# Optimization experiments

Measured on AMD Instinct MI355X. Metric: run time of the kernel, lower is better.

The kernel has to match this reference:

```python
import jax, jax.numpy as jnp
import numpy as np

NUM_LAYERS = 5
EMB = 300
N_GRAPHS = 4096
BN_EPS = 1e-5
TEMP = 0.04


def _gnn_encode(x, edge_index, edge_attr, atom_emb1, atom_emb2,
                edge_emb1, edge_emb2, mlp_w1, mlp_b1, mlp_w2, mlp_b2,
                bn_gamma, bn_beta):
    n = x.shape[0]
    h = atom_emb1[x[:, 0]] + atom_emb2[x[:, 1]]  # [N, EMB]
    src, dst = edge_index[0], edge_index[1]
    for l in range(NUM_LAYERS):
        eemb = edge_emb1[l][edge_attr[:, 0]] + edge_emb2[l][edge_attr[:, 1]]  # [E, EMB]
        self_emb = edge_emb1[l][4] + edge_emb2[l][0]  # self-loop edge_attr = [4, 0]
        agg = jax.ops.segment_sum(h[src] + eemb, dst, num_segments=n)
        agg = agg + h + self_emb  # self-loop messages
        h = jax.nn.relu(agg @ mlp_w1[l] + mlp_b1[l]) @ mlp_w2[l] + mlp_b2[l]
        mean = jnp.mean(h, axis=0)
        var = jnp.var(h, axis=0)
        h = (h - mean) / jnp.sqrt(var + BN_EPS) * bn_gamma[l] + bn_beta[l]
        if l != NUM_LAYERS - 1:
            h = jax.nn.relu(h)
    return h


def _branch(x, edge_index, edge_attr, node_batch, params):
    h = _gnn_encode(x, edge_index, edge_attr, *params[:-2])
    h = h @ params[-2] + params[-1]  # projector
    s = jax.ops.segment_sum(h, node_batch, num_segments=N_GRAPHS)
    cnt = jax.ops.segment_sum(jnp.ones((h.shape[0],), h.dtype), node_batch,
                              num_segments=N_GRAPHS)
    g = s / jnp.maximum(cnt, 1.0)[:, None]  # global mean pool
    norm = jnp.maximum(jnp.linalg.norm(g, axis=1, keepdims=True), 1e-12)
    return g / norm


def setup_inputs() -> dict:
    key = jax.random.key(0)
    ks = jax.random.split(key, 24)
    f = jnp.float32
    inp = {}
    inp['x0'] = jax.random.randint(ks[0], (100000, 2), 0, 3)
    inp['edge_index0'] = jax.random.randint(ks[1], (2, 400000), 0, 100000)
    inp['edge_attr0'] = jax.random.randint(ks[2], (400000, 2), 0, 3)
    inp['batch0'] = jnp.sort(jax.random.randint(ks[3], (100000,), 0, N_GRAPHS))
    inp['x1'] = jax.random.randint(ks[4], (100000, 2), 0, 3)
    inp['edge_index1'] = jax.random.randint(ks[5], (2, 400000), 0, 100000)
    inp['edge_attr1'] = jax.random.randint(ks[6], (400000, 2), 0, 3)
    inp['batch1'] = jnp.sort(jax.random.randint(ks[7], (100000,), 0, N_GRAPHS))
    s = 0.02
    inp['atom_emb1'] = jax.random.normal(ks[8], (120, EMB), f) * s
    inp['atom_emb2'] = jax.random.normal(ks[9], (3, EMB), f) * s
    inp['edge_emb1'] = jax.random.normal(ks[10], (NUM_LAYERS, 6, EMB), f) * s
    inp['edge_emb2'] = jax.random.normal(ks[11], (NUM_LAYERS, 3, EMB), f) * s
    inp['mlp_w1'] = jax.random.normal(ks[12], (NUM_LAYERS, EMB, 2 * EMB), f) * s
    inp['mlp_b1'] = jnp.zeros((NUM_LAYERS, 2 * EMB), f)
    inp['mlp_w2'] = jax.random.normal(ks[13], (NUM_LAYERS, 2 * EMB, EMB), f) * s
    inp['mlp_b2'] = jnp.zeros((NUM_LAYERS, EMB), f)
    inp['bn_gamma'] = jnp.ones((NUM_LAYERS, EMB), f)
    inp['bn_beta'] = jnp.zeros((NUM_LAYERS, EMB), f)
    inp['proj_w'] = jax.random.normal(ks[14], (EMB, EMB), f) * s
    inp['proj_b'] = jnp.zeros((EMB,), f)
    return inp


def reference(x0, edge_index0, edge_attr0, batch0,
              x1, edge_index1, edge_attr1, batch1,
              atom_emb1, atom_emb2, edge_emb1, edge_emb2,
              mlp_w1, mlp_b1, mlp_w2, mlp_b2, bn_gamma, bn_beta,
              proj_w, proj_b):
    params = (atom_emb1, atom_emb2, edge_emb1, edge_emb2,
              mlp_w1, mlp_b1, mlp_w2, mlp_b2, bn_gamma, bn_beta,
              proj_w, proj_b)
    f0 = _branch(x0, edge_index0, edge_attr0, batch0, params)
    f1 = _branch(x1, edge_index1, edge_attr1, batch1, params)
    logits = (f0 @ f1.T) / TEMP  # [G, G]
    return logits
```

## Files before the change

kernel.cpp:

```cpp
#include <hip/hip_runtime.h>
#include <hip/hip_bf16.h>


#define EMB 300
#define EMBC 75
#define AGGP 320
#define AGGC 80
#define HID 600
#define NGRAPH 4096
#define BN_EPS 1e-5f
#define INV_TEMP 25.0f

typedef __hip_bfloat16 bf16;
struct __align__(8) bf4 { bf16 x, y, z, w; };
typedef __attribute__((ext_vector_type(8))) short short8;
typedef __attribute__((ext_vector_type(4))) float float4v;

__device__ inline float b2f(bf16 v) { return __bfloat162float(v); }
__device__ inline bf16 f2b(float v) { return __float2bfloat16(v); }
__device__ inline unsigned short f2bu(float f) {
    bf16 b = __float2bfloat16(f); unsigned short u; __builtin_memcpy(&u, &b, 2); return u;
}

typedef const unsigned int __attribute__((address_space(1)))* gas_t;
typedef unsigned int __attribute__((address_space(3)))* las_t;
__device__ __forceinline__ void gl_lds16(const unsigned short* g, unsigned short* l) {
    __builtin_amdgcn_global_load_lds((gas_t)g, (las_t)l, 16, 0, 0);
}


__global__ void k_zero_f(float* __restrict__ p, int n) {
    int i = blockIdx.x * blockDim.x + threadIdx.x;
    if (i < n) p[i] = 0.f;
}
__global__ void k_zero_i(int* __restrict__ p, int n) {
    int i = blockIdx.x * blockDim.x + threadIdx.x;
    if (i < n) p[i] = 0;
}


__global__ void k_split(const float* __restrict__ W, int K, int N, int Kpad, int Npad,
                        unsigned short* __restrict__ hi, unsigned short* __restrict__ lo) {
    int idx = blockIdx.x * blockDim.x + threadIdx.x;
    if (idx >= Npad * Kpad) return;
    int n = idx / Kpad, k = idx % Kpad;
    float v = (n < N && k < K) ? W[(size_t)k * N + n] : 0.f;
    bf16 h = __float2bfloat16(v);
    float rem = v - __bfloat162float(h);
    bf16 l = __float2bfloat16(rem);
    unsigned short hu, lu;
    __builtin_memcpy(&hu, &h, 2); __builtin_memcpy(&lu, &l, 2);
    hi[idx] = hu; lo[idx] = lu;
}

__global__ void k_fsplit(const float* __restrict__ f, unsigned short* __restrict__ hi,
                         unsigned short* __restrict__ lo, int G) {
    int idx = blockIdx.x * blockDim.x + threadIdx.x;
    if (idx >= G * AGGP) return;
    int g = idx / AGGP, c = idx % AGGP;
    float v = (c < EMB) ? f[(size_t)g * EMB + c] : 0.f;
    bf16 h = __float2bfloat16(v);
    float rem = v - __bfloat162float(h);
    hi[idx] = f2bu(v) , hi[idx] = 0;
    unsigned short hu; __builtin_memcpy(&hu, &h, 2);
    hi[idx] = hu;
    lo[idx] = f2bu(rem);
}


__global__ void k_hist(const int* __restrict__ ei, int* __restrict__ deg, int E) {
    int e = blockIdx.x * blockDim.x + threadIdx.x;
    if (e < E) atomicAdd(&deg[ei[E + e]], 1);
}

__global__ void k_chunksum(const int* __restrict__ deg, int* __restrict__ csum, int total) {
    __shared__ int s[256];
    int t = threadIdx.x, i = blockIdx.x * 256 + t;
    s[t] = (i < total) ? deg[i] : 0;
    __syncthreads();
    for (int off = 128; off > 0; off >>= 1) {
        if (t < off) s[t] += s[t + off];
        __syncthreads();
    }
    if (t == 0) csum[blockIdx.x] = s[0];
}

__global__ void k_scanchunks(const int* __restrict__ csum, int* __restrict__ coff, int n) {
    if (threadIdx.x == 0) {
        int acc = 0;
        for (int b = 0; b < n; ++b) { coff[b] = acc; acc += csum[b]; }
    }
}

__global__ void k_scan2(const int* __restrict__ deg, const int* __restrict__ coff,
                        int* __restrict__ rowstart, int total) {
    __shared__ int s[256];
    int t = threadIdx.x, b = blockIdx.x, i = b * 256 + t;
    int v = (i < total) ? deg[i] : 0;
    s[t] = v;
    __syncthreads();
    for (int off = 1; off < 256; off <<= 1) {
        int u = (t >= off) ? s[t - off] : 0;
        __syncthreads();
        s[t] += u;
        __syncthreads();
    }
    if (i < total) rowstart[i] = coff[b] + s[t] - v;
}

__global__ void k_initcursor(const int* __restrict__ rowstart, int* __restrict__ cur, int N) {
    int i = blockIdx.x * blockDim.x + threadIdx.x;
    if (i < N) cur[i] = rowstart[i];
}

__global__ void k_fill(const int* __restrict__ ei, int* __restrict__ cur,
                       int* __restrict__ esorted, int E) {
    int e = blockIdx.x * blockDim.x + threadIdx.x;
    if (e < E) {
        int p = atomicAdd(&cur[ei[E + e]], 1);
        esorted[p] = e;
    }
}

__global__ void k_pack(const int* __restrict__ ei, const int* __restrict__ ea,
                       const int* __restrict__ esorted, int* __restrict__ packed, int E) {
    int p = blockIdx.x * blockDim.x + threadIdx.x;
    if (p >= E) return;
    int e = esorted[p];
    int s = ei[e];
    int cb = ea[2 * e] * 3 + ea[2 * e + 1];
    packed[p] = s | (cb << 17);
}

__global__ void k_gstart(const int* __restrict__ batch, int* __restrict__ gstart, int N) {
    int g = blockIdx.x * blockDim.x + threadIdx.x;
    if (g > NGRAPH) return;
    int lo = 0, hi = N;
    while (lo < hi) { int mid = (lo + hi) >> 1; if (batch[mid] < g) lo = mid + 1; else hi = mid; }
    gstart[g] = lo;
}

__global__ void k_combo(const float4* __restrict__ e1, const float4* __restrict__ e2,
                        float4* __restrict__ cmb) {
    int t = blockIdx.x * blockDim.x + threadIdx.x;
    if (t >= 18 * EMBC) return;
    int cb = t / EMBC, j = t % EMBC;
    float4 u = e1[(cb / 3) * EMBC + j];
    float4 v = e2[(cb % 3) * EMBC + j];
    float4 r; r.x = u.x + v.x; r.y = u.y + v.y; r.z = u.z + v.z; r.w = u.w + v.w;
    cmb[t] = r;
}


__global__ void k_init_h(const int* __restrict__ x,
                         const float4* __restrict__ ae1,
                         const float4* __restrict__ ae2,
                         bf4* __restrict__ h4, int N) {
    int idx = blockIdx.x * blockDim.x + threadIdx.x;
    if (idx >= N * EMBC) return;
    int i = idx / EMBC, j = idx % EMBC;
    int a0 = x[2 * i], a1 = x[2 * i + 1];
    float4 u = ae1[a0 * EMBC + j];
    float4 v = ae2[a1 * EMBC + j];
    bf4 r = { f2b(u.x + v.x), f2b(u.y + v.y), f2b(u.z + v.z), f2b(u.w + v.w) };
    h4[idx] = r;
}

__global__ void k_aggregate(const bf4* __restrict__ h4,
                            const int* __restrict__ packed,
                            const float4* __restrict__ cmb,
                            const int* __restrict__ rowstart,
                            const float* __restrict__ stats, int use_aff,
                            bf4* __restrict__ agg4, int N) {
    int idx = blockIdx.x * blockDim.x + threadIdx.x;
    if (idx >= N * AGGC) return;
    int n = idx / AGGC, j = idx % AGGC;
    if (j >= EMBC) {
        bf4 z = { f2b(0.f), f2b(0.f), f2b(0.f), f2b(0.f) };
        agg4[idx] = z;
        return;
    }
    float4 sc = make_float4(1.f, 1.f, 1.f, 1.f);
    float4 sh = make_float4(0.f, 0.f, 0.f, 0.f);
    if (use_aff) {
        sc = ((const float4*)stats)[j];
        sh = ((const float4*)(stats + EMB))[j];
    }
    bf4 hv = h4[(size_t)n * EMBC + j];
    float hx = b2f(hv.x), hy = b2f(hv.y), hz = b2f(hv.z), hw = b2f(hv.w);
    if (use_aff) {
        hx = fmaxf(hx * sc.x + sh.x, 0.f); hy = fmaxf(hy * sc.y + sh.y, 0.f);
        hz = fmaxf(hz * sc.z + sh.z, 0.f); hw = fmaxf(hw * sc.w + sh.w, 0.f);
    }
    float4 s0 = cmb[12 * EMBC + j];
    float ax = hx + s0.x, ay = hy + s0.y, az = hz + s0.z, aw = hw + s0.w;
    int p0 = rowstart[n], p1 = rowstart[n + 1];
    for (int p = p0; p < p1; ++p) {
        int u = packed[p];
        int s = u & 131071;
        int cb = u >> 17;
        bf4 hs = h4[(size_t)s * EMBC + j];
        float gx = b2f(hs.x), gy = b2f(hs.y), gz = b2f(hs.z), gw = b2f(hs.w);
        if (use_aff) {
            gx = fmaxf(gx * sc.x + sh.x, 0.f); gy = fmaxf(gy * sc.y + sh.y, 0.f);
            gz = fmaxf(gz * sc.z + sh.z, 0.f); gw = fmaxf(gw * sc.w + sh.w, 0.f);
        }
        float4 cv = cmb[cb * EMBC + j];
        ax += gx + cv.x; ay += gy + cv.y;
        az += gz + cv.z; aw += gw + cv.w;
    }
    bf4 r = { f2b(ax), f2b(ay), f2b(az), f2b(aw) };
    agg4[idx] = r;
}

__global__ void k_bncopy(const bf4* __restrict__ h4, const float* __restrict__ stats,
                         bf4* __restrict__ dst, int N) {
    int idx = blockIdx.x * blockDim.x + threadIdx.x;
    if (idx >= N * AGGC) return;
    int n = idx / AGGC, j = idx % AGGC;
    if (j >= EMBC) {
        bf4 z = { f2b(0.f), f2b(0.f), f2b(0.f), f2b(0.f) };
        dst[idx] = z;
        return;
    }
    float4 sc = ((const float4*)stats)[j];
    float4 sh = ((const float4*)(stats + EMB))[j];
    bf4 v = h4[(size_t)n * EMBC + j];
    bf4 r = { f2b(b2f(v.x) * sc.x + sh.x), f2b(b2f(v.y) * sc.y + sh.y),
              f2b(b2f(v.z) * sc.z + sh.z), f2b(b2f(v.w) * sc.w + sh.w) };
    dst[idx] = r;
}


#define GBM 128
#define GBN 128
#define GBK 64

__global__ __launch_bounds__(256)
void k_gemm_mfma(const unsigned short* __restrict__ A, int lda, int Kreal,
                 int Kpad, int Kasync,
                 const unsigned short* __restrict__ Bhi,
                 const unsigned short* __restrict__ Blo, int ldb,
                 const float* __restrict__ bias,
                 unsigned short* __restrict__ C, int ldc, int M, int Nc, int relu,
                 float* __restrict__ stats, int do_stats) {
    __shared__ unsigned short As[GBM][GBK];
    __shared__ unsigned short Bh[GBN][GBK];
    __shared__ unsigned short Bl[GBN][GBK];

    int tid = threadIdx.x;
    int wv = tid >> 6, lane = tid & 63;
    int quad = lane >> 4, l16 = lane & 15;
    int lrow = lane >> 3;
    int gchunk = (lane & 7) ^ lrow;
    int sw = lane & 7;
    int row0 = blockIdx.y * GBM;
    int col0 = blockIdx.x * GBN;

    float4v acc[2][8];
    #pragma unroll
    for (int i = 0; i < 2; ++i)
        #pragma unroll
        for (int j = 0; j < 8; ++j) acc[i][j] = (float4v){0.f, 0.f, 0.f, 0.f};

    for (int k0 = 0; k0 < Kpad; k0 += GBK) {
        if (k0 < Kasync) {
            #pragma unroll
            for (int j = 0; j < 4; ++j) {
                int r = 32 * wv + 8 * j + lrow;
                int gr = min(row0 + r, M - 1);
                gl_lds16(A + (size_t)gr * lda + k0 + gchunk * 8, &As[32 * wv + 8 * j][0]);
            }
            #pragma unroll
            for (int j = 0; j < 4; ++j) {
                int r = 32 * wv + 8 * j + lrow;
                size_t go = (size_t)(col0 + r) * ldb + k0 + gchunk * 8;
                gl_lds16(Bhi + go, &Bh[32 * wv + 8 * j][0]);
                gl_lds16(Blo + go, &Bl[32 * wv + 8 * j][0]);
            }
        } else {
            #pragma unroll
            for (int i = 0; i < 4; ++i) {
                int cidx = tid + i * 256;
                int r = cidx >> 3, s = cidx & 7;
                int g = s ^ (r & 7);
                int gr = min(row0 + r, M - 1);
                unsigned short tmp[8];
                #pragma unroll
                for (int t = 0; t < 8; ++t) {
                    int gk = k0 + g * 8 + t;
                    tmp[t] = (gk < Kreal) ? A[(size_t)gr * lda + gk] : (unsigned short)0;
                }
                uint4 w; __builtin_memcpy(&w, tmp, 16);
                *(uint4*)(&As[r][s * 8]) = w;
            }
            #pragma unroll
            for (int j = 0; j < 4; ++j) {
                int r = 32 * wv + 8 * j + lrow;
                size_t go = (size_t)(col0 + r) * ldb + k0 + gchunk * 8;
                gl_lds16(Bhi + go, &Bh[32 * wv + 8 * j][0]);
                gl_lds16(Blo + go, &Bl[32 * wv + 8 * j][0]);
            }
        }
        __syncthreads();

        int mbase = wv * 32;
        #pragma unroll
        for (int ks = 0; ks < GBK; ks += 32) {
            int lc = (ks >> 3) + quad;
            int pc = lc ^ sw;
            short8 a0 = *(const short8*)(&As[mbase + l16][pc * 8]);
            short8 a1 = *(const short8*)(&As[mbase + 16 + l16][pc * 8]);
            #pragma unroll
            for (int nt = 0; nt < 8; ++nt) {
                short8 bh = *(const short8*)(&Bh[nt * 16 + l16][pc * 8]);
                short8 bl = *(const short8*)(&Bl[nt * 16 + l16][pc * 8]);
                acc[0][nt] = __builtin_amdgcn_mfma_f32_16x16x32_bf16(a0, bh, acc[0][nt], 0, 0, 0);
                acc[0][nt] = __builtin_amdgcn_mfma_f32_16x16x32_bf16(a0, bl, acc[0][nt], 0, 0, 0);
                acc[1][nt] = __builtin_amdgcn_mfma_f32_16x16x32_bf16(a1, bh, acc[1][nt], 0, 0, 0);
                acc[1][nt] = __builtin_amdgcn_mfma_f32_16x16x32_bf16(a1, bl, acc[1][nt], 0, 0, 0);
            }
        }
        __syncthreads();
    }

    float sv[8], qv[8];
    #pragma unroll
    for (int nt = 0; nt < 8; ++nt) { sv[nt] = 0.f; qv[nt] = 0.f; }
    #pragma unroll
    for (int mt = 0; mt < 2; ++mt) {
        int rbase = row0 + wv * 32 + mt * 16 + quad * 4;
        #pragma unroll
        for (int nt = 0; nt < 8; ++nt) {
            int c = col0 + nt * 16 + l16;
            if (c >= Nc) continue;
            float bs = bias[c];
            #pragma unroll
            for (int i = 0; i < 4; ++i) {
                int r = rbase + i;
                if (r >= M) continue;
                float v = acc[mt][nt][i] + bs;
                if (relu) v = fmaxf(v, 0.f);
                if (do_stats) { sv[nt] += v; qv[nt] += v * v; }
                C[(size_t)r * ldc + c] = f2bu(v);
            }
        }
    }
    if (do_stats) {
        float* cred = (float*)(&As[0][0]);
        #pragma unroll
        for (int nt = 0; nt < 8; ++nt) {
            float s = sv[nt], q = qv[nt];
            s += __shfl_down(s, 32, 64); s += __shfl_down(s, 16, 64);
            q += __shfl_down(q, 32, 64); q += __shfl_down(q, 16, 64);
            if (quad == 0) {
                cred[(wv * 2 + 0) * 128 + nt * 16 + l16] = s;
                cred[(wv * 2 + 1) * 128 + nt * 16 + l16] = q;
            }
        }
        __syncthreads();
        if (tid < 128) {
            int c = col0 + tid;
            if (c < Nc) {
                float s = cred[0 * 128 + tid] + cred[2 * 128 + tid] +
                          cred[4 * 128 + tid] + cred[6 * 128 + tid];
                float q = cred[1 * 128 + tid] + cred[3 * 128 + tid] +
                          cred[5 * 128 + tid] + cred[7 * 128 + tid];
                atomicAdd(&stats[c], s);
                atomicAdd(&stats[EMB + c], q);
            }
        }
    }
}


__global__ __launch_bounds__(256)
void k_logits(const unsigned short* __restrict__ Ahg, const unsigned short* __restrict__ Alg,
              const unsigned short* __restrict__ Bhg, const unsigned short* __restrict__ Blg,
              float* __restrict__ C, float scale) {
    __shared__ unsigned short sAh[64][64];
    __shared__ unsigned short sAl[64][64];
    __shared__ unsigned short sBh[128][64];
    __shared__ unsigned short sBl[128][64];

    int tid = threadIdx.x;
    int wv = tid >> 6, lane = tid & 63;
    int quad = lane >> 4, l16 = lane & 15;
    int lrow = lane >> 3;
    int gchunk = (lane & 7) ^ lrow;
    int sw = lane & 7;
    int row0 = blockIdx.y * 64;
    int col0 = blockIdx.x * 128;

    float4v acc[8];
    #pragma unroll
    for (int j = 0; j < 8; ++j) acc[j] = (float4v){0.f, 0.f, 0.f, 0.f};

    for (int k0 = 0; k0 < AGGP; k0 += 64) {
        #pragma unroll
        for (int j = 0; j < 2; ++j) {
            int r = 16 * wv + 8 * j + lrow;
            size_t go = (size_t)(row0 + r) * AGGP + k0 + gchunk * 8;
            gl_lds16(Ahg + go, &sAh[16 * wv + 8 * j][0]);
            gl_lds16(Alg + go, &sAl[16 * wv + 8 * j][0]);
        }
        #pragma unroll
        for (int j = 0; j < 4; ++j) {
            int r = 32 * wv + 8 * j + lrow;
            size_t go = (size_t)(col0 + r) * AGGP + k0 + gchunk * 8;
            gl_lds16(Bhg + go, &sBh[32 * wv + 8 * j][0]);
            gl_lds16(Blg + go, &sBl[32 * wv + 8 * j][0]);
        }
        __syncthreads();

        #pragma unroll
        for (int ks = 0; ks < 64; ks += 32) {
            int pc = ((ks >> 3) + quad) ^ sw;
            short8 ah = *(const short8*)(&sAh[wv * 16 + l16][pc * 8]);
            short8 al = *(const short8*)(&sAl[wv * 16 + l16][pc * 8]);
            #pragma unroll
            for (int nt = 0; nt < 8; ++nt) {
                short8 bh = *(const short8*)(&sBh[nt * 16 + l16][pc * 8]);
                short8 bl = *(const short8*)(&sBl[nt * 16 + l16][pc * 8]);
                acc[nt] = __builtin_amdgcn_mfma_f32_16x16x32_bf16(ah, bh, acc[nt], 0, 0, 0);
                acc[nt] = __builtin_amdgcn_mfma_f32_16x16x32_bf16(ah, bl, acc[nt], 0, 0, 0);
                acc[nt] = __builtin_amdgcn_mfma_f32_16x16x32_bf16(al, bh, acc[nt], 0, 0, 0);
            }
        }
        __syncthreads();
    }

    int rbase = row0 + wv * 16 + quad * 4;
    #pragma unroll
    for (int nt = 0; nt < 8; ++nt) {
        int c = col0 + nt * 16 + l16;
        #pragma unroll
        for (int i = 0; i < 4; ++i)
            C[(size_t)(rbase + i) * NGRAPH + c] = acc[nt][i] * scale;
    }
}


__global__ void k_bn_prep(float* __restrict__ stats, const float* __restrict__ gamma,
                          const float* __restrict__ beta, float invN) {
    int c = threadIdx.x;
    if (c >= EMB) return;
    float mean = stats[c] * invN;
    float var = stats[EMB + c] * invN - mean * mean;
    float scale = gamma[c] * rsqrtf(var + BN_EPS);
    stats[c] = scale;
    stats[EMB + c] = beta[c] - mean * scale;
}


__global__ void k_poolnorm(const bf16* __restrict__ proj, const int* __restrict__ gstart,
                           float* __restrict__ f) {
    int g = blockIdx.x, t = threadIdx.x;
    int s = gstart[g], e = gstart[g + 1];
    float sum = 0.f;
    if (t < EMB)
        for (int r = s; r < e; ++r) sum += b2f(proj[(size_t)r * AGGP + t]);
    float cnt = fmaxf((float)(e - s), 1.f);
    float m = sum / cnt;
    float q = (t < EMB) ? m * m : 0.f;
    for (int off = 32; off > 0; off >>= 1) q += __shfl_down(q, off, 64);
    __shared__ float red[5];
    int lane = t & 63, wid = t >> 6;
    if (lane == 0) red[wid] = q;
    __syncthreads();
    float tot = red[0] + red[1] + red[2] + red[3] + red[4];
    float invn = 1.f / fmaxf(sqrtf(tot), 1e-12f);
    if (t < EMB) f[(size_t)g * EMB + t] = m * invn;
}


static inline int ceil_div(int a, int b) { return (a + b - 1) / b; }

extern "C" void kernel_launch(void* const* d_in, const int* in_sizes, int n_in,
                              void* d_out, int out_size, void* d_ws, size_t ws_size,
                              hipStream_t stream) {
    const int N = in_sizes[0] / 2;
    const int E = in_sizes[1] / 2;

    const int* x[2]  = { (const int*)d_in[0], (const int*)d_in[4] };
    const int* ei[2] = { (const int*)d_in[1], (const int*)d_in[5] };
    const int* ea[2] = { (const int*)d_in[2], (const int*)d_in[6] };
    const int* bt[2] = { (const int*)d_in[3], (const int*)d_in[7] };
    const float* atom1 = (const float*)d_in[8];
    const float* atom2 = (const float*)d_in[9];
    const float* ee1 = (const float*)d_in[10];
    const float* ee2 = (const float*)d_in[11];
    const float* w1  = (const float*)d_in[12];
    const float* b1  = (const float*)d_in[13];
    const float* w2  = (const float*)d_in[14];
    const float* b2  = (const float*)d_in[15];
    const float* gam = (const float*)d_in[16];
    const float* bet = (const float*)d_in[17];
    const float* pw  = (const float*)d_in[18];
    const float* pb  = (const float*)d_in[19];
    float* out = (float*)d_out;

    char* wsb = (char*)d_ws;
    bf16* h    = (bf16*)(wsb);
    bf16* agg  = (bf16*)(wsb + 60000000);
    bf16* hid  = (bf16*)(wsb + 124000000);
    float* f0  = (float*)(wsb + 244000000);
    float* f1  = (float*)(wsb + 248915200);
    unsigned short* f0hi = (unsigned short*)(wsb + 124000000);
    unsigned short* f0lo = (unsigned short*)(wsb + 126621440);
    unsigned short* f1hi = (unsigned short*)(wsb + 129242880);
    unsigned short* f1lo = (unsigned short*)(wsb + 131864320);

    int* deg      = (int*)d_out;
    int* rowstart = deg + (N + 1);
    int* cursor   = rowstart + (N + 1);
    int* esorted  = cursor + N;
    int* packed   = esorted + E;
    int* csum     = packed + E;
    int* coff     = csum + 512;
    int* gstart   = coff + 512;
    float* stats  = (float*)(gstart + 4097);
    float* cmb    = stats + 600;
    char* splits  = (char*)d_out + 4500224;
    unsigned short* w1hi = (unsigned short*)(splits);
    unsigned short* w1lo = (unsigned short*)(splits + 2048000);
    unsigned short* w2hi = (unsigned short*)(splits + 4096000);
    unsigned short* w2lo = (unsigned short*)(splits + 6553600);
    unsigned short* pjhi = (unsigned short*)(splits + 9011200);
    unsigned short* pjlo = (unsigned short*)(splits + 9256960);

    const int TB = 256;
    const int nh_blocks = ceil_div(N * EMBC, TB);
    const int na_blocks = ceil_div(N * AGGC, TB);
    const int nchunks = ceil_div(N + 1, 256);
    const float invN = 1.f / (float)N;

    for (int l = 0; l < 5; ++l) {
        k_split<<<ceil_div(640 * 320, TB), TB, 0, stream>>>(
            w1 + (size_t)l * EMB * HID, EMB, HID, 320, 640,
            w1hi + (size_t)l * 640 * 320, w1lo + (size_t)l * 640 * 320);
        k_split<<<ceil_div(384 * 640, TB), TB, 0, stream>>>(
            w2 + (size_t)l * HID * EMB, HID, EMB, 640, 384,
            w2hi + (size_t)l * 384 * 640, w2lo + (size_t)l * 384 * 640);
    }
    k_split<<<ceil_div(384 * 320, TB), TB, 0, stream>>>(pw, EMB, EMB, 320, 384, pjhi, pjlo);

    const int mrows = ceil_div(N, GBM);
    dim3 g1(5, mrows);
    dim3 g2(3, mrows);
    dim3 glg(32, 64);

    for (int br = 0; br < 2; ++br) {
        float* fout = br == 0 ? f0 : f1;
        k_zero_i<<<ceil_div(N + 1, TB), TB, 0, stream>>>(deg, N + 1);
        k_hist<<<ceil_div(E, TB), TB, 0, stream>>>(ei[br], deg, E);
        k_chunksum<<<nchunks, 256, 0, stream>>>(deg, csum, N + 1);
        k_scanchunks<<<1, 64, 0, stream>>>(csum, coff, nchunks);
        k_scan2<<<nchunks, 256, 0, stream>>>(deg, coff, rowstart, N + 1);
        k_initcursor<<<ceil_div(N, TB), TB, 0, stream>>>(rowstart, cursor, N);
        k_fill<<<ceil_div(E, TB), TB, 0, stream>>>(ei[br], cursor, esorted, E);
        k_pack<<<ceil_div(E, TB), TB, 0, stream>>>(ei[br], ea[br], esorted, packed, E);
        k_gstart<<<ceil_div(NGRAPH + 1, TB), TB, 0, stream>>>(bt[br], gstart, N);
        k_init_h<<<nh_blocks, TB, 0, stream>>>(x[br], (const float4*)atom1,
                                               (const float4*)atom2, (bf4*)h, N);
        for (int l = 0; l < 5; ++l) {
            k_combo<<<ceil_div(18 * EMBC, TB), TB, 0, stream>>>(
                (const float4*)(ee1 + (size_t)l * 6 * EMB),
                (const float4*)(ee2 + (size_t)l * 3 * EMB), (float4*)cmb);
            k_aggregate<<<na_blocks, TB, 0, stream>>>((const bf4*)h, packed,
                                                      (const float4*)cmb, rowstart,
                                                      stats, l > 0, (bf4*)agg, N);
            k_gemm_mfma<<<g1, 256, 0, stream>>>(
                (const unsigned short*)agg, AGGP, AGGP, AGGP, AGGP,
                w1hi + (size_t)l * 640 * 320, w1lo + (size_t)l * 640 * 320, 320,
                b1 + (size_t)l * HID, (unsigned short*)hid, HID, N, HID, 1,
                nullptr, 0);
            k_zero_f<<<ceil_div(2 * EMB, TB), TB, 0, stream>>>(stats, 2 * EMB);
            k_gemm_mfma<<<g2, 256, 0, stream>>>(
                (const unsigned short*)hid, HID, HID, 640, 576,
                w2hi + (size_t)l * 384 * 640, w2lo + (size_t)l * 384 * 640, 640,
                b2 + (size_t)l * EMB, (unsigned short*)h, EMB, N, EMB, 0,
                stats, 1);
            k_bn_prep<<<1, 320, 0, stream>>>(stats, gam + (size_t)l * EMB,
                                             bet + (size_t)l * EMB, invN);
        }
        k_bncopy<<<na_blocks, TB, 0, stream>>>((const bf4*)h, stats, (bf4*)hid, N);
        k_gemm_mfma<<<g2, 256, 0, stream>>>(
            (const unsigned short*)hid, AGGP, AGGP, AGGP, AGGP,
            pjhi, pjlo, 320, pb, (unsigned short*)agg, AGGP, N, EMB, 0,
            nullptr, 0);
        k_poolnorm<<<NGRAPH, 320, 0, stream>>>(agg, gstart, fout);
    }
    k_fsplit<<<ceil_div(NGRAPH * AGGP, TB), TB, 0, stream>>>(f0, f0hi, f0lo, NGRAPH);
    k_fsplit<<<ceil_div(NGRAPH * AGGP, TB), TB, 0, stream>>>(f1, f1hi, f1lo, NGRAPH);
    k_logits<<<glg, 256, 0, stream>>>(f0hi, f0lo, f1hi, f1lo, out, INV_TEMP);
}
```

Baseline: 4.462 ms.

## Use 2x2 warp tiling and grouped block order in MFMA GEMM

Result: faster. 4.209 ms (-5.7%).

```diff
diff --git a/kernel.cpp b/kernel.cpp
--- a/kernel.cpp
+++ b/kernel.cpp
@@ -61,7 +61,6 @@
     float v = (c < EMB) ? f[(size_t)g * EMB + c] : 0.f;
     bf16 h = __float2bfloat16(v);
     float rem = v - __bfloat162float(h);
-    hi[idx] = f2bu(v) , hi[idx] = 0;
     unsigned short hu; __builtin_memcpy(&hu, &h, 2);
     hi[idx] = hu;
     lo[idx] = f2bu(rem);
@@ -251,17 +250,26 @@
     int tid = threadIdx.x;
     int wv = tid >> 6, lane = tid & 63;
     int quad = lane >> 4, l16 = lane & 15;
+    int wm = wv & 1, wn = wv >> 1;
     int lrow = lane >> 3;
     int gchunk = (lane & 7) ^ lrow;
     int sw = lane & 7;
-    int row0 = blockIdx.y * GBM;
-    int col0 = blockIdx.x * GBN;
-
-    float4v acc[2][8];
+
+    int ncols = gridDim.x, nrows = gridDim.y;
+    int lin = blockIdx.y * ncols + blockIdx.x;
+    int g = lin / (8 * ncols);
+    int rem = lin - g * 8 * ncols;
+    int rows_in = min(8, nrows - g * 8);
+    int colb = rem / rows_in;
+    int rowb = g * 8 + (rem - colb * rows_in);
+    int row0 = rowb * GBM;
+    int col0 = colb * GBN;
+
+    float4v acc[4][4];
     #pragma unroll
-    for (int i = 0; i < 2; ++i)
-        #pragma unroll
-        for (int j = 0; j < 8; ++j) acc[i][j] = (float4v){0.f, 0.f, 0.f, 0.f};
+    for (int i = 0; i < 4; ++i)
+        #pragma unroll
+        for (int j = 0; j < 4; ++j) acc[i][j] = (float4v){0.f, 0.f, 0.f, 0.f};
 
     for (int k0 = 0; k0 < Kpad; k0 += GBK) {
         if (k0 < Kasync) {
@@ -283,12 +291,12 @@
             for (int i = 0; i < 4; ++i) {
                 int cidx = tid + i * 256;
                 int r = cidx >> 3, s = cidx & 7;
-                int g = s ^ (r & 7);
+                int gg = s ^ (r & 7);
                 int gr = min(row0 + r, M - 1);
                 unsigned short tmp[8];
                 #pragma unroll
                 for (int t = 0; t < 8; ++t) {
-                    int gk = k0 + g * 8 + t;
+                    int gk = k0 + gg * 8 + t;
                     tmp[t] = (gk < Kreal) ? A[(size_t)gr * lda + gk] : (unsigned short)0;
                 }
                 uint4 w; __builtin_memcpy(&w, tmp, 16);
@@ -304,35 +312,37 @@
         }
         __syncthreads();
 
-        int mbase = wv * 32;
+        int mbase = wm * 64, nbase = wn * 64;
         #pragma unroll
         for (int ks = 0; ks < GBK; ks += 32) {
-            int lc = (ks >> 3) + quad;
-            int pc = lc ^ sw;
-            short8 a0 = *(const short8*)(&As[mbase + l16][pc * 8]);
-            short8 a1 = *(const short8*)(&As[mbase + 16 + l16][pc * 8]);
-            #pragma unroll
-            for (int nt = 0; nt < 8; ++nt) {
-                short8 bh = *(const short8*)(&Bh[nt * 16 + l16][pc * 8]);
-                short8 bl = *(const short8*)(&Bl[nt * 16 + l16][pc * 8]);
-                acc[0][nt] = __builtin_amdgcn_mfma_f32_16x16x32_bf16(a0, bh, acc[0][nt], 0, 0, 0);
-                acc[0][nt] = __builtin_amdgcn_mfma_f32_16x16x32_bf16(a0, bl, acc[0][nt], 0, 0, 0);
-                acc[1][nt] = __builtin_amdgcn_mfma_f32_16x16x32_bf16(a1, bh, acc[1][nt], 0, 0, 0);
-                acc[1][nt] = __builtin_amdgcn_mfma_f32_16x16x32_bf16(a1, bl, acc[1][nt], 0, 0, 0);
-            }
-        }
-        __syncthreads();
-    }
-
-    float sv[8], qv[8];
+            int pc = ((ks >> 3) + quad) ^ sw;
+            short8 a[4];
+            #pragma unroll
+            for (int mt = 0; mt < 4; ++mt)
+                a[mt] = *(const short8*)(&As[mbase + mt * 16 + l16][pc * 8]);
+            #pragma unroll
+            for (int nt = 0; nt < 4; ++nt) {
+                short8 bh = *(const short8*)(&Bh[nbase + nt * 16 + l16][pc * 8]);
+                short8 bl = *(const short8*)(&Bl[nbase + nt * 16 + l16][pc * 8]);
+                #pragma unroll
+                for (int mt = 0; mt < 4; ++mt) {
+                    acc[mt][nt] = __builtin_amdgcn_mfma_f32_16x16x32_bf16(a[mt], bh, acc[mt][nt], 0, 0, 0);
+                    acc[mt][nt] = __builtin_amdgcn_mfma_f32_16x16x32_bf16(a[mt], bl, acc[mt][nt], 0, 0, 0);
+                }
+            }
+        }
+        __syncthreads();
+    }
+
+    float sv[4], qv[4];
     #pragma unroll
-    for (int nt = 0; nt < 8; ++nt) { sv[nt] = 0.f; qv[nt] = 0.f; }
+    for (int nt = 0; nt < 4; ++nt) { sv[nt] = 0.f; qv[nt] = 0.f; }
     #pragma unroll
-    for (int mt = 0; mt < 2; ++mt) {
-        int rbase = row0 + wv * 32 + mt * 16 + quad * 4;
-        #pragma unroll
-        for (int nt = 0; nt < 8; ++nt) {
-            int c = col0 + nt * 16 + l16;
+    for (int mt = 0; mt < 4; ++mt) {
+        int rbase = row0 + wm * 64 + mt * 16 + quad * 4;
+        #pragma unroll
+        for (int nt = 0; nt < 4; ++nt) {
+            int c = col0 + wn * 64 + nt * 16 + l16;
             if (c >= Nc) continue;
             float bs = bias[c];
             #pragma unroll
@@ -349,23 +359,22 @@
     if (do_stats) {
         float* cred = (float*)(&As[0][0]);
         #pragma unroll
-        for (int nt = 0; nt < 8; ++nt) {
+        for (int nt = 0; nt < 4; ++nt) {
             float s = sv[nt], q = qv[nt];
             s += __shfl_down(s, 32, 64); s += __shfl_down(s, 16, 64);
             q += __shfl_down(q, 32, 64); q += __shfl_down(q, 16, 64);
             if (quad == 0) {
-                cred[(wv * 2 + 0) * 128 + nt * 16 + l16] = s;
-                cred[(wv * 2 + 1) * 128 + nt * 16 + l16] = q;
+                cred[wv * 128 + nt * 16 + l16] = s;
+                cred[wv * 128 + 64 + nt * 16 + l16] = q;
             }
         }
         __syncthreads();
         if (tid < 128) {
             int c = col0 + tid;
             if (c < Nc) {
-                float s = cred[0 * 128 + tid] + cred[2 * 128 + tid] +
-                          cred[4 * 128 + tid] + cred[6 * 128 + tid];
-                float q = cred[1 * 128 + tid] + cred[3 * 128 + tid] +
-                          cred[5 * 128 + tid] + cred[7 * 128 + tid];
+                int cin = tid & 63, wvn = tid >> 6;
+                float s = cred[(wvn * 2 + 0) * 128 + cin] + cred[(wvn * 2 + 1) * 128 + cin];
+                float q = cred[(wvn * 2 + 0) * 128 + 64 + cin] + cred[(wvn * 2 + 1) * 128 + 64 + cin];
                 atomicAdd(&stats[c], s);
                 atomicAdd(&stats[EMB + c], q);
             }
@@ -504,8 +513,9 @@
     bf16* h    = (bf16*)(wsb);
     bf16* agg  = (bf16*)(wsb + 60000000);
     bf16* hid  = (bf16*)(wsb + 124000000);
-    float* f0  = (float*)(wsb + 244000000);
-    float* f1  = (float*)(wsb + 248915200);
+    float* guard = (float*)(wsb + 244000000);
+    float* f0  = (float*)(wsb + 244000256);
+    float* f1  = (float*)(wsb + 248915456);
     unsigned short* f0hi = (unsigned short*)(wsb + 124000000);
     unsigned short* f0lo = (unsigned short*)(wsb + 126621440);
     unsigned short* f1hi = (unsigned short*)(wsb + 129242880);
@@ -534,6 +544,8 @@
     const int na_blocks = ceil_div(N * AGGC, TB);
     const int nchunks = ceil_div(N + 1, 256);
     const float invN = 1.f / (float)N;
+
+    k_zero_f<<<1, 64, 0, stream>>>(guard, 64);
 
     for (int l = 0; l < 5; ++l) {
         k_split<<<ceil_div(640 * 320, TB), TB, 0, stream>>>(
@@ -577,7 +589,7 @@
                 nullptr, 0);
             k_zero_f<<<ceil_div(2 * EMB, TB), TB, 0, stream>>>(stats, 2 * EMB);
             k_gemm_mfma<<<g2, 256, 0, stream>>>(
-                (const unsigned short*)hid, HID, HID, 640, 576,
+                (const unsigned short*)hid, HID, HID, 640, 640,
                 w2hi + (size_t)l * 384 * 640, w2lo + (size_t)l * 384 * 640, 640,
                 b2 + (size_t)l * EMB, (unsigned short*)h, EMB, N, EMB, 0,
                 stats, 1);
```
